# Kernel optimization log

Measured on AMD Instinct MI355X. Metric: run time of the kernel, lower is better.

## Reference

```python
import jax, jax.numpy as jnp
import numpy as np

N_VARS = 1_000_000
N_CLAUSES = 4_000_000
N_EDGES = 12_000_000


def setup_inputs() -> dict:
    key = jax.random.key(0)
    k1, k2, k3 = jax.random.split(key, 3)
    preds = jax.random.uniform(k1, (N_VARS,), dtype=jnp.float32)
    lits = jax.random.randint(k2, (N_EDGES,), 0, 2 * N_VARS, dtype=jnp.int32)
    clauses = jax.random.randint(k3, (N_EDGES,), 0, N_CLAUSES, dtype=jnp.int32)
    return {
        "preds": preds,
        "lits": lits,
        "clauses": clauses,
        "n_vars": N_VARS,
        "n_clauses": N_CLAUSES,
    }


def reference(preds, lits, clauses, n_vars, n_clauses):
    # Map literal index to variable index: lits < n_vars -> positive literal,
    # lits >= n_vars -> negated literal of variable (lits - n_vars).
    is_pos = lits < n_vars
    var_idx = jnp.where(is_pos, lits, lits - n_vars)
    pval = preds[var_idx]                                   # gather [n_edges]
    # positive literal satisfied if pred >= 0.5, negated if pred < 0.5
    satisfied = jnp.where(is_pos, pval >= 0.5, pval < 0.5).astype(jnp.float32)
    # scatter-add satisfaction flags into per-clause bins, then threshold to bool
    clause_hits = jax.ops.segment_sum(satisfied, clauses, num_segments=n_clauses)
    clause_sat = clause_hits > 0                            # [n_clauses] bool
    n_sat = clause_sat.sum().astype(jnp.float32)
    loss = (jnp.float32(n_clauses) - n_sat) / jnp.float32(n_vars)
    return loss
```

## Files before the change

kernel.cpp:

```cpp
#include <hip/hip_runtime.h>
#include <stdint.h>

#define BLOCK 256

typedef int iv4 __attribute__((ext_vector_type(4)));


__global__ void prep(const float* __restrict__ preds,
                     unsigned long long* __restrict__ predbits,
                     uint4* __restrict__ satz,
                     unsigned* __restrict__ hdr,
                     int n_vars,
                     const int* __restrict__ nc_p) {
    const int gid = blockIdx.x * blockDim.x + threadIdx.x;
    const int stride = gridDim.x * blockDim.x;

    const int nv64 = (n_vars + 63) & ~63;
    for (int i = gid; i < nv64; i += stride) {
        bool b = false;
        if (i < n_vars) b = (__builtin_nontemporal_load(&preds[i]) >= 0.5f);
        const unsigned long long m = __ballot(b);
        if ((threadIdx.x & 63) == 0) predbits[i >> 6] = m;
    }

    const int nc = *nc_p;
    const int satw16 = (nc + 15) >> 4;
    const uint4 z = {0u, 0u, 0u, 0u};
    for (int i = gid; i < satw16; i += stride) satz[i] = z;

    if (gid == 0) { hdr[0] = 0u; hdr[1] = 0u; }
}

__device__ __forceinline__ void edge_one(int lit, int cls, int nv,
                                         const unsigned* __restrict__ predbits,
                                         unsigned char* __restrict__ sat) {
    const bool pos = lit < nv;
    const int v = pos ? lit : lit - nv;
    const unsigned pb = predbits[v >> 5];
    const bool pbit = ((pb >> (v & 31)) & 1u) != 0u;
    if (pbit == pos) sat[cls] = (unsigned char)1;
}

__global__ void scatter_sat(const int* __restrict__ lits,
                            const int* __restrict__ clauses,
                            const unsigned* __restrict__ predbits,
                            unsigned char* __restrict__ sat,
                            int n_edges, int n_vars) {
    const int tid = blockIdx.x * blockDim.x + threadIdx.x;
    const int stride = gridDim.x * blockDim.x;
    const int n4 = n_edges >> 2;

    const iv4* __restrict__ l4 = reinterpret_cast<const iv4*>(lits);
    const iv4* __restrict__ c4 = reinterpret_cast<const iv4*>(clauses);

    for (int i = tid; i < n4; i += stride) {
        const iv4 l = __builtin_nontemporal_load(&l4[i]);
        const iv4 c = __builtin_nontemporal_load(&c4[i]);
        edge_one(l.x, c.x, n_vars, predbits, sat);
        edge_one(l.y, c.y, n_vars, predbits, sat);
        edge_one(l.z, c.z, n_vars, predbits, sat);
        edge_one(l.w, c.w, n_vars, predbits, sat);
    }
    for (int i = (n4 << 2) + tid; i < n_edges; i += stride) {
        edge_one(lits[i], clauses[i], n_vars, predbits, sat);
    }
}

__global__ void reduce_finalize(const uint4* __restrict__ sat16,
                                unsigned* __restrict__ nsat,
                                unsigned* __restrict__ done,
                                float* __restrict__ out,
                                const int* __restrict__ nc_p,
                                int n_vars) {
    const int nc = *nc_p;
    const int n16 = (nc + 15) >> 4;
    const int tid = blockIdx.x * blockDim.x + threadIdx.x;
    const int stride = gridDim.x * blockDim.x;

    unsigned acc = 0;
    for (int i = tid; i < n16; i += stride) {
        const uint4 v = sat16[i];
        acc += __popc(v.x & 0x01010101u) + __popc(v.y & 0x01010101u) +
               __popc(v.z & 0x01010101u) + __popc(v.w & 0x01010101u);
    }

    #pragma unroll
    for (int off = 32; off > 0; off >>= 1) acc += __shfl_down(acc, off);

    __shared__ unsigned smem[BLOCK / 64];
    const int lane = threadIdx.x & 63;
    const int wid  = threadIdx.x >> 6;
    if (lane == 0) smem[wid] = acc;
    __syncthreads();

    if (threadIdx.x == 0) {
        unsigned bsum = 0;
        #pragma unroll
        for (int w = 0; w < BLOCK / 64; ++w) bsum += smem[w];
        atomicAdd(nsat, bsum);
        __threadfence();
        const unsigned ticket = atomicAdd(done, 1u);
        if (ticket == (unsigned)(gridDim.x - 1)) {
            const unsigned total = atomicAdd(nsat, 0u);
            *out = ((float)nc - (float)total) / (float)n_vars;
        }
    }
}

extern "C" void kernel_launch(void* const* d_in, const int* in_sizes, int n_in,
                              void* d_out, int out_size, void* d_ws, size_t ws_size,
                              hipStream_t stream) {
    const float* preds   = (const float*)d_in[0];
    const int*   lits    = (const int*)d_in[1];
    const int*   clauses = (const int*)d_in[2];
    const int*   nc_p    = (const int*)d_in[4];
    const int    n_vars  = in_sizes[0];
    const int    n_edges = in_sizes[1];

    float* out = (float*)d_out;
    unsigned char* ws = (unsigned char*)d_ws;
    unsigned* hdr = (unsigned*)ws;
    unsigned long long* predbits = (unsigned long long*)(ws + 64);
    const size_t predbits_bytes = ((size_t)((n_vars + 63) / 64)) * 8;
    size_t satoff = 64 + predbits_bytes;
    satoff = (satoff + 63) & ~(size_t)63;
    unsigned char* sat = ws + satoff;

    prep<<<2048, BLOCK, 0, stream>>>(preds, predbits, (uint4*)sat, hdr,
                                     n_vars, nc_p);
    scatter_sat<<<2048, BLOCK, 0, stream>>>(lits, clauses,
                                            (const unsigned*)predbits, sat,
                                            n_edges, n_vars);
    reduce_finalize<<<256, BLOCK, 0, stream>>>((const uint4*)sat,
                                               hdr, hdr + 1, out, nc_p, n_vars);
}
```

Measured before the change: 272.9 us.

## Partition clause scatter by XCD so each die pair owns a clause range

```diff
diff --git a/kernel.cpp b/kernel.cpp
--- a/kernel.cpp
+++ b/kernel.cpp
@@ -2,6 +2,8 @@
 #include <stdint.h>
 
 #define BLOCK 256
+#define NPART 4
+#define CHUNK 8192
 
 typedef int iv4 __attribute__((ext_vector_type(4)));
 
@@ -28,41 +30,66 @@
     const uint4 z = {0u, 0u, 0u, 0u};
     for (int i = gid; i < satw16; i += stride) satz[i] = z;
 
-    if (gid == 0) { hdr[0] = 0u; hdr[1] = 0u; }
-}
-
-__device__ __forceinline__ void edge_one(int lit, int cls, int nv,
-                                         const unsigned* __restrict__ predbits,
-                                         unsigned char* __restrict__ sat) {
-    const bool pos = lit < nv;
-    const int v = pos ? lit : lit - nv;
-    const unsigned pb = predbits[v >> 5];
-    const bool pbit = ((pb >> (v & 31)) & 1u) != 0u;
-    if (pbit == pos) sat[cls] = (unsigned char)1;
+    if (gid < 8) hdr[gid] = 0u;
 }
 
 __global__ void scatter_sat(const int* __restrict__ lits,
                             const int* __restrict__ clauses,
                             const unsigned* __restrict__ predbits,
                             unsigned char* __restrict__ sat,
-                            int n_edges, int n_vars) {
-    const int tid = blockIdx.x * blockDim.x + threadIdx.x;
-    const int stride = gridDim.x * blockDim.x;
-    const int n4 = n_edges >> 2;
+                            unsigned* __restrict__ cursors,
+                            int n_edges, int n_vars,
+                            const int* __restrict__ nc_p) {
+    unsigned xcd;
+    asm volatile("s_getreg_b32 %0, hwreg(HW_REG_XCC_ID)" : "=s"(xcd));
+    const unsigned part = (xcd & 7u) >> 1;
+
+    const int nc = *nc_p;
+    const unsigned psize = (unsigned)((nc + NPART - 1) / NPART);
+    const unsigned lo = part * psize;
 
     const iv4* __restrict__ l4 = reinterpret_cast<const iv4*>(lits);
     const iv4* __restrict__ c4 = reinterpret_cast<const iv4*>(clauses);
 
-    for (int i = tid; i < n4; i += stride) {
-        const iv4 l = __builtin_nontemporal_load(&l4[i]);
-        const iv4 c = __builtin_nontemporal_load(&c4[i]);
-        edge_one(l.x, c.x, n_vars, predbits, sat);
-        edge_one(l.y, c.y, n_vars, predbits, sat);
-        edge_one(l.z, c.z, n_vars, predbits, sat);
-        edge_one(l.w, c.w, n_vars, predbits, sat);
-    }
-    for (int i = (n4 << 2) + tid; i < n_edges; i += stride) {
-        edge_one(lits[i], clauses[i], n_vars, predbits, sat);
+    __shared__ unsigned s_base;
+    for (;;) {
+        if (threadIdx.x == 0)
+            s_base = atomicAdd(&cursors[part], (unsigned)CHUNK);
+        __syncthreads();
+        const unsigned base = s_base;
+        __syncthreads();
+        if (base >= (unsigned)n_edges) break;
+        const unsigned end = min(base + (unsigned)CHUNK, (unsigned)n_edges);
+
+        const int i4b = base >> 2;
+        const int i4e = end >> 2;
+        for (int i = i4b + (int)threadIdx.x; i < i4e; i += BLOCK) {
+            const iv4 l = __builtin_nontemporal_load(&l4[i]);
+            const iv4 c = __builtin_nontemporal_load(&c4[i]);
+            #pragma unroll
+            for (int k = 0; k < 4; ++k) {
+                const int lit = l[k];
+                const int cls = c[k];
+                if ((unsigned)cls - lo < psize) {
+                    const bool pos = lit < n_vars;
+                    const int v = pos ? lit : lit - n_vars;
+                    const unsigned pb = predbits[v >> 5];
+                    const bool pbit = ((pb >> (v & 31)) & 1u) != 0u;
+                    if (pbit == pos) sat[cls] = (unsigned char)1;
+                }
+            }
+        }
+        for (unsigned i = (unsigned)(i4e << 2) + threadIdx.x; i < end; i += BLOCK) {
+            const int lit = lits[i];
+            const int cls = clauses[i];
+            if ((unsigned)cls - lo < psize) {
+                const bool pos = lit < n_vars;
+                const int v = pos ? lit : lit - n_vars;
+                const unsigned pb = predbits[v >> 5];
+                const bool pbit = ((pb >> (v & 31)) & 1u) != 0u;
+                if (pbit == pos) sat[cls] = (unsigned char)1;
+            }
+        }
     }
 }
 
@@ -130,7 +157,7 @@
                                      n_vars, nc_p);
     scatter_sat<<<2048, BLOCK, 0, stream>>>(lits, clauses,
                                             (const unsigned*)predbits, sat,
-                                            n_edges, n_vars);
+                                            hdr + 2, n_edges, n_vars, nc_p);
     reduce_finalize<<<256, BLOCK, 0, stream>>>((const uint4*)sat,
                                                hdr, hdr + 1, out, nc_p, n_vars);
 }
```

After: 422.3 us. +54.7%, slower.
